# Kernel tuning notes

Hardware: AMD Instinct MI355X
Metric: run time of the kernel (lower is better)

## Reference

```python
import jax, jax.numpy as jnp
import numpy as np

B, T = 32, 64
I, O, H = 64, 64, 512
N, W = 128, 64           # memory slots, slot width
IF = 3 * W + 6           # interface size


def setup_inputs() -> dict:
    key = jax.random.key(0)
    ks = jax.random.split(key, 6)
    s = 0.05
    return {
        "x": jax.random.normal(ks[0], (B, T, I), jnp.float32),
        "W_ih": jax.random.normal(ks[1], (4 * H, I + W), jnp.float32) * s,
        "W_hh": jax.random.normal(ks[2], (4 * H, H), jnp.float32) * s,
        "b_ih": jnp.zeros((4 * H,), jnp.float32),
        "b_hh": jnp.zeros((4 * H,), jnp.float32),
        "W_if": jax.random.normal(ks[3], (IF, H), jnp.float32) * s,
        "b_if": jnp.zeros((IF,), jnp.float32),
        "W_out": jax.random.normal(ks[4], (O, H + W), jnp.float32) * s,
        "b_out": jnp.zeros((O,), jnp.float32),
    }


def reference(x, W_ih, W_hh, b_ih, b_hh, W_if, b_if, W_out, b_out):
    Bb, Tt, _ = x.shape
    dt = x.dtype
    eye = jnp.eye(N, dtype=dt)
    batch_idx = jnp.arange(Bb)[:, None]

    def step(carry, x_t):
        h, c, mem, usage, prec, link, rw, rvec = carry
        # --- LSTM controller (PyTorch gate order i,f,g,o) ---
        inp = jnp.concatenate([x_t, rvec], axis=-1)
        gates = inp @ W_ih.T + h @ W_hh.T + b_ih + b_hh
        i_g, f_g, g_g, o_g = jnp.split(gates, 4, axis=-1)
        c = jax.nn.sigmoid(f_g) * c + jax.nn.sigmoid(i_g) * jnp.tanh(g_g)
        h = jax.nn.sigmoid(o_g) * jnp.tanh(c)
        itf = h @ W_if.T + b_if
        # --- parse interface ---
        erase = jax.nn.sigmoid(itf[:, :W])
        wvec = itf[:, W:2 * W]
        wg = jax.nn.sigmoid(itf[:, 2 * W])
        ag = jax.nn.sigmoid(itf[:, 2 * W + 1])
        rstr = jnp.log1p(jnp.exp(itf[:, 3 * W + 2]))  # softplus
        # --- allocation weighting (sort usage asc, shifted cumprod, scatter) ---
        idx = jnp.argsort(usage, axis=-1)
        usage_sorted = jnp.take_along_axis(usage, idx, axis=-1)
        cprod = jnp.cumprod(usage_sorted, axis=-1)
        cprod = jnp.concatenate([jnp.ones((Bb, 1), dt), cprod[:, :-1]], axis=-1)
        alloc_in_order = (1.0 - usage_sorted) * cprod
        alloc = jnp.zeros_like(usage).at[batch_idx, idx].set(alloc_in_order)
        ww = wg[:, None] * ag[:, None] * alloc  # [B,N]
        # --- erase + add write ---
        mem = mem * (1.0 - ww[:, :, None] * erase[:, None, :]) + ww[:, :, None] * wvec[:, None, :]
        usage = usage + (1.0 - usage) * ww
        # --- temporal link / precedence ---
        ww_ij = ww[:, :, None] + ww[:, None, :]
        link = (1.0 - ww_ij) * link + prec[:, :, None] * ww[:, None, :]
        link = link * (1.0 - eye)
        prec = (1.0 - ww.sum(-1, keepdims=True)) * prec + ww
        # --- read weights (NOTE: source uses itf[:, :W] as read key) ---
        rmode = jax.nn.softmax(itf[:, -3:], axis=-1)
        rkey = itf[:, :W]
        dot = jnp.einsum('bw,bnw->bn', rkey, mem)
        kn = jnp.linalg.norm(rkey, axis=-1, keepdims=True) + 1e-8
        mn = jnp.linalg.norm(mem, axis=-1) + 1e-8
        cw = jax.nn.softmax(dot / (kn * mn) * rstr[:, None], axis=-1)
        bw = jnp.einsum('bnm,bn->bm', link, rw)   # link^T @ rw
        fw = jnp.einsum('bnm,bm->bn', link, rw)   # link @ rw
        wts = rmode[:, 0:1] * bw + rmode[:, 1:2] * fw + rmode[:, 2:3] * cw + 1e-8
        wts = wts / wts.sum(-1, keepdims=True)
        rvec = jnp.einsum('bn,bnw->bw', wts, mem)
        out = jnp.concatenate([h, rvec], axis=-1) @ W_out.T + b_out
        return (h, c, mem, usage, prec, link, wts, rvec), out

    z = lambda *s: jnp.zeros(s, dt)
    carry0 = (z(Bb, H), z(Bb, H), z(Bb, N, W), z(Bb, N), z(Bb, N), z(Bb, N, N), z(Bb, N), z(Bb, W))
    _, outs = jax.lax.scan(step, carry0, jnp.swapaxes(x, 0, 1))
    return jnp.swapaxes(outs, 0, 1)  # [B,T,O]
```

## Files before the change

### kernel.cpp

```cpp
#include <hip/hip_runtime.h>
#include <math.h>

#define Bb 32
#define Tt 64
#define Ii 64
#define Oo 64
#define Hh 512
#define Nn 128
#define Wd 64
#define IFs 198
#define KV 640
#define G4 2048

#define NP1 128
#define NWG 160
#define NT 512

#define P2_MEM    0
#define P2_H      8320
#define P2_SCR    8896
#define P2_ITF    10944
#define P2_ERASE  11168
#define P2_WVEC   11232
#define P2_USAGE  11296
#define P2_PREC   11424
#define P2_RW     11552
#define P2_WW     11680
#define P2_SCAN   11808
#define P2_SS     11936
#define P2_SCAL   12064
#define P2_BIF    12080
#define P2_ALLOC  12304
#define P1_WIF    0
#define P1_BS     13464
#define P1_V      13720
#define P1_CC     15016
#define P1_HSL    15144
#define P1_PACC   15272
#define SMEM_FLOATS 23592
#define SMEM_BYTES (SMEM_FLOATS * 4)

#define S_WWSUM 0

__device__ __align__(16) float g_WT[KV * G4];
__device__ __align__(16) float g_bsum[G4];
typedef unsigned long long u64;
__device__ u64 g_h64[2 * Bb * Hh];
__device__ u64 g_rv64[Bb * Wd];
__device__ u64 g_if64[Bb * 8 * 200];

__device__ __forceinline__ float sigf(float v) { return 1.f / (1.f + expf(-v)); }

__device__ __forceinline__ u64 ldrelax(const u64* p) {
  return __hip_atomic_load(p, __ATOMIC_RELAXED, __HIP_MEMORY_SCOPE_AGENT);
}
__device__ __forceinline__ void tstore(u64* p, unsigned tag, float v) {
  u64 val = ((u64)tag << 32) | (u64)__float_as_uint(v);
  __hip_atomic_store(p, val, __ATOMIC_RELAXED, __HIP_MEMORY_SCOPE_AGENT);
}
__device__ __forceinline__ float fixwait(const u64* p, u64 v, unsigned tag) {
  while ((unsigned)(v >> 32) != tag) {
    __builtin_amdgcn_s_sleep(1);
    v = ldrelax(p);
  }
  return __uint_as_float((unsigned)(v & 0xffffffffu));
}

#define TIN 512
__global__ __launch_bounds__(TIN) void dnc_init(const float* __restrict__ W_ih,
                                                const float* __restrict__ W_hh,
                                                const float* __restrict__ b_ih,
                                                const float* __restrict__ b_hh) {
  __shared__ float tile[64][65];
  const int tid = threadIdx.x;
  int i0 = blockIdx.x * blockDim.x + tid;
  int st = gridDim.x * blockDim.x;
  for (int idx = i0; idx < G4; idx += st) g_bsum[idx] = b_ih[idx] + b_hh[idx];
  for (int idx = i0; idx < 2 * Bb * Hh; idx += st) g_h64[idx] = 0ull;
  for (int idx = i0; idx < Bb * Wd; idx += st) g_rv64[idx] = 0ull;
  for (int idx = i0; idx < Bb * 8 * 200; idx += st) g_if64[idx] = 0ull;

  for (int tileId = blockIdx.x; tileId < 320; tileId += gridDim.x) {
    int tc = tileId >> 5, tj = tileId & 31;
    for (int k = tid; k < 64 * 64; k += TIN) {
      int r = k >> 6, cl = k & 63;
      int j = tj * 64 + r, c = tc * 64 + cl;
      tile[r][cl] = (c < 128) ? W_ih[j * 128 + c] : W_hh[j * 512 + (c - 128)];
    }
    __syncthreads();
    for (int k = tid; k < 64 * 64; k += TIN) {
      int cl = k >> 6, rjj = k & 63;
      int c = tc * 64 + cl;
      int rp = (c < 128) ? (512 + c) : (c - 128);
      g_WT[(size_t)rp * G4 + tj * 64 + rjj] = tile[rjj][cl];
    }
    __syncthreads();
  }
}

__global__ __launch_bounds__(NT) void dnc_main(const float* __restrict__ x,
                                               const float* __restrict__ W_if,
                                               const float* __restrict__ b_if,
                                               const float* __restrict__ W_out,
                                               const float* __restrict__ b_out,
                                               float* __restrict__ out) {
  extern __shared__ float sm[];
  const int tid = threadIdx.x;
  const int wg = blockIdx.x;

  if (wg < NP1) {
    const int jb = wg & 7;
    const int bb = wg >> 3;
    const int b0 = bb * 2;
    for (int i = tid; i < IFs * 64; i += NT) {
      int o = i >> 6, c = i & 63;
      sm[P1_WIF + o * 68 + c] = W_if[(size_t)o * Hh + jb * 64 + c];
    }
    if (tid < 64) {
      int gq = tid >> 4, m = tid & 15;
      ((float4*)(sm + P1_BS))[tid] = ((const float4*)g_bsum)[gq * 128 + jb * 16 + m];
    }
    if (tid < 128) sm[P1_CC + tid] = 0.f;
    __syncthreads();

    for (int t = 0; t < Tt; ++t) {
      {
        const u64* hsrc = g_h64 + (size_t)((t + 1) & 1) * (Bb * Hh);
        const int u = tid;
        const u64* a0 = hsrc + (size_t)b0 * Hh + u;
        const u64* a1 = hsrc + (size_t)(b0 + 1) * Hh + u;
        u64 v0 = ldrelax(a0), v1 = ldrelax(a1);
        float2 hh;
        hh.x = fixwait(a0, v0, (unsigned)t);
        hh.y = fixwait(a1, v1, (unsigned)t);
        *(float2*)(sm + P1_V + u * 2) = hh;
        if (tid < 128) {
          const int bl2 = tid >> 6, i = tid & 63;
          float xv = x[((size_t)(b0 + bl2) * Tt + t) * Ii + i];
          sm[P1_V + (512 + i) * 2 + bl2] = xv;
        }
      }
      __syncthreads();

      {
        const int fg = tid & 31, ks = tid >> 5;
        const int fcolA = ((fg >> 4) * 128) + jb * 16 + (fg & 15);
        const float* v2 = sm + P1_V + ks * 80;
        const float4* wpA = (const float4*)g_WT + (size_t)(ks * 40) * 512 + fcolA;
        if (ks >= 14) {
          const int j = tid & 63;
          const u64* r0 = g_rv64 + (size_t)b0 * Wd + j;
          const u64* r1 = g_rv64 + (size_t)(b0 + 1) * Wd + j;
          u64 u0 = ldrelax(r0), u1 = ldrelax(r1);
          float2 rv;
          rv.x = fixwait(r0, u0, (unsigned)t);
          rv.y = fixwait(r1, u1, (unsigned)t);
          *(float2*)(sm + P1_V + (576 + j) * 2) = rv;
        }
        float4 aA0 = {0.f, 0.f, 0.f, 0.f}, aA1 = {0.f, 0.f, 0.f, 0.f};
        float4 aB0 = {0.f, 0.f, 0.f, 0.f}, aB1 = {0.f, 0.f, 0.f, 0.f};
#pragma unroll 4
        for (int r = 0; r < 40; ++r) {
          float4 wA = wpA[(size_t)r * 512];
          float4 wB = wpA[(size_t)r * 512 + 256];
          float2 vv = *(const float2*)(v2 + r * 2);
          aA0.x += wA.x * vv.x; aA0.y += wA.y * vv.x; aA0.z += wA.z * vv.x; aA0.w += wA.w * vv.x;
          aA1.x += wA.x * vv.y; aA1.y += wA.y * vv.y; aA1.z += wA.z * vv.y; aA1.w += wA.w * vv.y;
          aB0.x += wB.x * vv.x; aB0.y += wB.y * vv.x; aB0.z += wB.z * vv.x; aB0.w += wB.w * vv.x;
          aB1.x += wB.x * vv.y; aB1.y += wB.y * vv.y; aB1.z += wB.z * vv.y; aB1.w += wB.w * vv.y;
        }
        float4* pacc = (float4*)(sm + P1_PACC);
        pacc[(ks * 2 + 0) * 65 + fg] = aA0;
        pacc[(ks * 2 + 1) * 65 + fg] = aA1;
        pacc[(ks * 2 + 0) * 65 + fg + 32] = aB0;
        pacc[(ks * 2 + 1) * 65 + fg + 32] = aB1;
      }
      __syncthreads();
      if (tid < 128) {
        const int bl = tid >> 6, l = tid & 63;
        const float* pb = sm + P1_PACC + bl * 260 + l;
        float gv0 = 0.f, gv1 = 0.f, gv2 = 0.f, gv3 = 0.f;
#pragma unroll
        for (int ks = 0; ks < 16; ++ks) {
          const float* pk = pb + ks * 520;
          gv0 += pk[0];
          gv1 += pk[64];
          gv2 += pk[128];
          gv3 += pk[192];
        }
        float ig = gv0 + sm[P1_BS + l];
        float fg = gv1 + sm[P1_BS + 64 + l];
        float gg = gv2 + sm[P1_BS + 128 + l];
        float og = gv3 + sm[P1_BS + 192 + l];
        float co = sm[P1_CC + bl * 64 + l];
        float cn = sigf(fg) * co + sigf(ig) * tanhf(gg);
        float hn = sigf(og) * tanhf(cn);
        sm[P1_CC + bl * 64 + l] = cn;
        sm[P1_HSL + bl * 64 + l] = hn;
        tstore(g_h64 + (size_t)(t & 1) * (Bb * Hh) + (size_t)(b0 + bl) * Hh + jb * 64 + l,
               (unsigned)(t + 1), hn);
      }
      __syncthreads();
      if (tid < 2 * IFs) {
        const int o = tid >> 1, bl = tid & 1;
        const float4* wr = (const float4*)(sm + P1_WIF + o * 68);
        const float4* h4 = (const float4*)(sm + P1_HSL + bl * 64);
        float acc = 0.f;
#pragma unroll 8
        for (int c4 = 0; c4 < 16; ++c4) {
          float4 w = wr[c4]; float4 h = h4[c4];
          acc += w.x * h.x + w.y * h.y + w.z * h.z + w.w * h.w;
        }
        tstore(g_if64 + ((size_t)(b0 + bl) * 8 + jb) * 200 + o, (unsigned)(t + 1), acc);
      }
    }
  } else {
    const int b = wg - NP1;
    float* SCR = sm + P2_SCR;
    float regL[32], regLT[32];
#pragma unroll
    for (int k = 0; k < 32; ++k) { regL[k] = 0.f; regLT[k] = 0.f; }
    for (int i = tid; i < Nn * 65; i += NT) sm[P2_MEM + i] = 0.f;
    if (tid < 128) { sm[P2_USAGE + tid] = 0.f; sm[P2_PREC + tid] = 0.f; sm[P2_RW + tid] = 0.f; }
    if (tid < IFs) sm[P2_BIF + tid] = b_if[tid];
    __syncthreads();
    if (tid < 64) {
      const int li = tid, i0 = 2 * li, i1 = i0 + 1;
      float u0 = sm[P2_USAGE + i0], u1 = sm[P2_USAGE + i1];
      int r0 = 0, r1 = 0;
      for (int jc = 0; jc < 32; ++jc) {
        float4 uj4 = *(const float4*)(sm + P2_USAGE + jc * 4);
#pragma unroll
        for (int e = 0; e < 4; ++e) {
          float uj = (&uj4.x)[e];
          int j = jc * 4 + e;
          r0 += (uj < u0 || (uj == u0 && j < i0)) ? 1 : 0;
          r1 += (uj < u1 || (uj == u1 && j < i1)) ? 1 : 0;
        }
      }
      sm[P2_SS + r0] = u0;
      sm[P2_SS + r1] = u1;
      float s0 = sm[P2_SS + i0], s1 = sm[P2_SS + i1];
      float p = s0 * s1;
#pragma unroll
      for (int off = 1; off < 64; off <<= 1) {
        float v = __shfl_up(p, off, 64);
        if (li >= off) p *= v;
      }
      float E = __shfl_up(p, 1, 64);
      if (li == 0) E = 1.f;
      sm[P2_SCAN + i0] = E * s0;
      sm[P2_SCAN + i1] = E * s0 * s1;
      float ex0 = (r0 > 0) ? sm[P2_SCAN + r0 - 1] : 1.f;
      float ex1 = (r1 > 0) ? sm[P2_SCAN + r1 - 1] : 1.f;
      sm[P2_ALLOC + i0] = (1.f - u0) * ex0;
      sm[P2_ALLOC + i1] = (1.f - u1) * ex1;
    }
    __syncthreads();

    for (int t = 0; t < Tt; ++t) {
      if (tid < 2 * IFs) {
        const int o = tid >> 1, hf = tid & 1;
        const u64* src = g_if64 + ((size_t)b * 8 + hf * 4) * 200 + o;
        u64 a0 = ldrelax(src), a1 = ldrelax(src + 200),
            a2 = ldrelax(src + 400), a3 = ldrelax(src + 600);
        float s = fixwait(src, a0, (unsigned)(t + 1))
                + fixwait(src + 200, a1, (unsigned)(t + 1))
                + fixwait(src + 400, a2, (unsigned)(t + 1))
                + fixwait(src + 600, a3, (unsigned)(t + 1));
        s += __shfl_xor(s, 1, 64);
        if (hf == 0) sm[P2_ITF + o] = s + sm[P2_BIF + o];
      }
      __syncthreads();
      float kn_r = 0.f, rstr_r = 0.f, rm0_r = 0.f, rm1_r = 0.f, rm2_r = 0.f;
      if (tid < 64) {
        const int li = tid, i0 = 2 * li, i1 = i0 + 1;
        float wgag = sigf(sm[P2_ITF + 128]) * sigf(sm[P2_ITF + 129]);
        float rs = sm[P2_ITF + 194];
        rstr_r = (rs > 20.f) ? rs : log1pf(expf(rs));
        float m0 = sm[P2_ITF + 195], m1 = sm[P2_ITF + 196], m2 = sm[P2_ITF + 197];
        float mx = fmaxf(m0, fmaxf(m1, m2));
        float e0 = expf(m0 - mx), e1 = expf(m1 - mx), e2 = expf(m2 - mx);
        float es = e0 + e1 + e2;
        rm0_r = e0 / es; rm1_r = e1 / es; rm2_r = e2 / es;
        float rk = sm[P2_ITF + li];
        sm[P2_ERASE + li] = sigf(rk);
        sm[P2_WVEC + li] = sm[P2_ITF + 64 + li];
        float sq = rk * rk;
#pragma unroll
        for (int off = 32; off > 0; off >>= 1) sq += __shfl_xor(sq, off, 64);
        kn_r = sqrtf(sq) + 1e-8f;
        float u0 = sm[P2_USAGE + i0], u1 = sm[P2_USAGE + i1];
        float w0 = wgag * sm[P2_ALLOC + i0];
        float w1 = wgag * sm[P2_ALLOC + i1];
        sm[P2_WW + i0] = w0; sm[P2_WW + i1] = w1;
        sm[P2_USAGE + i0] = u0 + (1.f - u0) * w0;
        sm[P2_USAGE + i1] = u1 + (1.f - u1) * w1;
        float wws = w0 + w1;
#pragma unroll
        for (int off = 32; off > 0; off >>= 1) wws += __shfl_xor(wws, off, 64);
        if (li == 0) sm[P2_SCAL + S_WWSUM] = wws;
      }
      __syncthreads();
      {
        const int n = tid & 127, ws = tid >> 7;
        float4 er[4], wv[4], kf[4];
#pragma unroll
        for (int r = 0; r < 4; ++r) {
          er[r] = *(const float4*)(sm + P2_ERASE + ws * 16 + r * 4);
          wv[r] = *(const float4*)(sm + P2_WVEC + ws * 16 + r * 4);
          kf[r] = *(const float4*)(sm + P2_ITF + ws * 16 + r * 4);
        }
        float wwn = sm[P2_WW + n];
        float dotp = 0.f, mnp = 0.f;
        const int base = P2_MEM + n * 65 + ws * 16;
#pragma unroll
        for (int q = 0; q < 16; ++q) {
          float m = sm[base + q];
          float ee = (&er[q >> 2].x)[q & 3];
          float vv = (&wv[q >> 2].x)[q & 3];
          float kk = (&kf[q >> 2].x)[q & 3];
          m = m * (1.f - wwn * ee) + wwn * vv;
          sm[base + q] = m;
          dotp += kk * m;
          mnp += m * m;
        }
        SCR[ws * 128 + n] = dotp;
        SCR[512 + ws * 128 + n] = mnp;
        const int m = n, ns = ws;
        float wwm = wwn;
        float prn = sm[P2_PREC + m];
        float bwp = 0.f, fwp = 0.f;
#pragma unroll
        for (int kq = 0; kq < 8; ++kq) {
          float4 ww4 = *(const float4*)(sm + P2_WW + ns * 32 + kq * 4);
          float4 pr4 = *(const float4*)(sm + P2_PREC + ns * 32 + kq * 4);
          float4 rw4 = *(const float4*)(sm + P2_RW + ns * 32 + kq * 4);
#pragma unroll
          for (int e = 0; e < 4; ++e) {
            int k = kq * 4 + e;
            int nn = ns * 32 + k;
            float wwo = (&ww4.x)[e];
            float pro = (&pr4.x)[e];
            float rwo = (&rw4.x)[e];
            float L = regL[k];
            L = (1.f - wwo - wwm) * L + pro * wwm;
            if (nn == m) L = 0.f;
            regL[k] = L;
            bwp += L * rwo;
            float LT = regLT[k];
            LT = (1.f - wwm - wwo) * LT + prn * wwo;
            if (nn == m) LT = 0.f;
            regLT[k] = LT;
            fwp += LT * rwo;
          }
        }
        SCR[1024 + ns * 128 + m] = bwp;
        SCR[1536 + ns * 128 + m] = fwp;
      }
      __syncthreads();
      if (tid < 64) {
        int i0 = 2 * tid, i1 = i0 + 1;
        float d0 = SCR[i0] + SCR[128 + i0] + SCR[256 + i0] + SCR[384 + i0];
        float d1 = SCR[i1] + SCR[128 + i1] + SCR[256 + i1] + SCR[384 + i1];
        float mn0 = sqrtf(SCR[512 + i0] + SCR[640 + i0] + SCR[768 + i0] + SCR[896 + i0]) + 1e-8f;
        float mn1 = sqrtf(SCR[512 + i1] + SCR[640 + i1] + SCR[768 + i1] + SCR[896 + i1]) + 1e-8f;
        float bw0 = SCR[1024 + i0] + SCR[1152 + i0] + SCR[1280 + i0] + SCR[1408 + i0];
        float bw1 = SCR[1024 + i1] + SCR[1152 + i1] + SCR[1280 + i1] + SCR[1408 + i1];
        float fw0 = SCR[1536 + i0] + SCR[1664 + i0] + SCR[1792 + i0] + SCR[1920 + i0];
        float fw1 = SCR[1536 + i1] + SCR[1664 + i1] + SCR[1792 + i1] + SCR[1920 + i1];
        float q0 = d0 / (kn_r * mn0) * rstr_r;
        float q1 = d1 / (kn_r * mn1) * rstr_r;
        float mx = fmaxf(q0, q1);
#pragma unroll
        for (int off = 32; off > 0; off >>= 1) mx = fmaxf(mx, __shfl_xor(mx, off, 64));
        float e0 = expf(q0 - mx), e1 = expf(q1 - mx);
        float es = e0 + e1;
#pragma unroll
        for (int off = 32; off > 0; off >>= 1) es += __shfl_xor(es, off, 64);
        float wv0 = rm0_r * bw0 + rm1_r * fw0 + rm2_r * (e0 / es) + 1e-8f;
        float wv1 = rm0_r * bw1 + rm1_r * fw1 + rm2_r * (e1 / es) + 1e-8f;
        float wsum = wv0 + wv1;
#pragma unroll
        for (int off = 32; off > 0; off >>= 1) wsum += __shfl_xor(wsum, off, 64);
        sm[P2_RW + i0] = wv0 / wsum;
        sm[P2_RW + i1] = wv1 / wsum;
      }
      __syncthreads();
      {
        const int w = tid & 63, ns8 = tid >> 6;
        float4 rw4[4];
#pragma unroll
        for (int r = 0; r < 4; ++r)
          rw4[r] = *(const float4*)(sm + P2_RW + ns8 * 16 + r * 4);
        float p = 0.f;
#pragma unroll
        for (int k = 0; k < 16; ++k)
          p += (&rw4[k >> 2].x)[k & 3] * sm[P2_MEM + (ns8 * 16 + k) * 65 + w];
        SCR[ns8 * 64 + w] = p;
      }
      __syncthreads();
      if (tid < 64) {
        float r = 0.f;
#pragma unroll
        for (int s2 = 0; s2 < 8; ++s2) r += SCR[s2 * 64 + tid];
        sm[P2_H + 512 + tid] = r;
        tstore(g_rv64 + (size_t)b * Wd + tid, (unsigned)(t + 1), r);
      } else if (tid < 320) {
        const int idx = tid - 64;
        const u64* hsrc = g_h64 + (size_t)(t & 1) * (Bb * Hh) + (size_t)b * Hh;
        const u64* a0 = hsrc + idx * 2;
        const u64* a1 = hsrc + idx * 2 + 1;
        u64 v0 = ldrelax(a0), v1 = ldrelax(a1);
        sm[P2_H + idx * 2] = fixwait(a0, v0, (unsigned)(t + 1));
        sm[P2_H + idx * 2 + 1] = fixwait(a1, v1, (unsigned)(t + 1));
      } else if (tid < 384) {
        const int li = tid - 320, i0 = 2 * li, i1 = i0 + 1;
        float u0 = sm[P2_USAGE + i0], u1 = sm[P2_USAGE + i1];
        int r0 = 0, r1 = 0;
        for (int jc = 0; jc < 32; ++jc) {
          float4 uj4 = *(const float4*)(sm + P2_USAGE + jc * 4);
#pragma unroll
          for (int e = 0; e < 4; ++e) {
            float uj = (&uj4.x)[e];
            int j = jc * 4 + e;
            r0 += (uj < u0 || (uj == u0 && j < i0)) ? 1 : 0;
            r1 += (uj < u1 || (uj == u1 && j < i1)) ? 1 : 0;
          }
        }
        sm[P2_SS + r0] = u0;
        sm[P2_SS + r1] = u1;
        float s0 = sm[P2_SS + i0], s1 = sm[P2_SS + i1];
        float p = s0 * s1;
#pragma unroll
        for (int off = 1; off < 64; off <<= 1) {
          float v = __shfl_up(p, off, 64);
          if (li >= off) p *= v;
        }
        float E = __shfl_up(p, 1, 64);
        if (li == 0) E = 1.f;
        sm[P2_SCAN + i0] = E * s0;
        sm[P2_SCAN + i1] = E * s0 * s1;
        float ex0 = (r0 > 0) ? sm[P2_SCAN + r0 - 1] : 1.f;
        float ex1 = (r1 > 0) ? sm[P2_SCAN + r1 - 1] : 1.f;
        sm[P2_ALLOC + i0] = (1.f - u0) * ex0;
        sm[P2_ALLOC + i1] = (1.f - u1) * ex1;
      } else {
        const int n = tid - 384;
        float wws = sm[P2_SCAL + S_WWSUM];
        sm[P2_PREC + n] = (1.f - wws) * sm[P2_PREC + n] + sm[P2_WW + n];
      }
      __syncthreads();
      {
        const int o = tid >> 3, seg = tid & 7;
        const float4* wrow = (const float4*)(W_out + (size_t)o * 576) + seg * 18;
        const float4* hb = (const float4*)(sm + P2_H) + seg * 18;
        float p = 0.f;
#pragma unroll
        for (int q = 0; q < 18; ++q) {
          float4 w = wrow[q]; float4 h = hb[q];
          p += w.x * h.x + w.y * h.y + w.z * h.z + w.w * h.w;
        }
        p += __shfl_down(p, 4, 8);
        p += __shfl_down(p, 2, 8);
        p += __shfl_down(p, 1, 8);
        if (seg == 0) out[((size_t)b * Tt + t) * Oo + o] = p + b_out[o];
      }
    }
  }
}

extern "C" void kernel_launch(void* const* d_in, const int* in_sizes, int n_in,
                              void* d_out, int out_size, void* d_ws, size_t ws_size,
                              hipStream_t stream) {
  (void)in_sizes; (void)n_in; (void)d_ws; (void)ws_size; (void)out_size;
  const float* x    = (const float*)d_in[0];
  const float* W_ih = (const float*)d_in[1];
  const float* W_hh = (const float*)d_in[2];
  const float* b_ih = (const float*)d_in[3];
  const float* b_hh = (const float*)d_in[4];
  const float* W_if = (const float*)d_in[5];
  const float* b_if = (const float*)d_in[6];
  const float* W_out = (const float*)d_in[7];
// ... 14 lines not shown
```

Baseline: 873.5 us.

## Merge memory-phase workgroups into LSTM workgroups with redundant per-batch memory state

The separate 32 memory-phase workgroups are removed. Each of the 128 controller workgroups now redundantly keeps the DNC memory, usage, precedence and link state for its two batch rows in LDS and registers. This drops the read-vector round trip through global memory and one cross-workgroup handoff per step, leaving only the h and interface-partial exchanges. The output projection is split across the 8 column workgroups and deferred by one step. In exchange, the memory update is computed eight times over, LDS use per workgroup grows, and the link matrix lives in large per-thread register arrays that may spill.

Result: slower. 2.089 ms (+139.1%).

```diff
diff --git a/kernel.cpp b/kernel.cpp
--- a/kernel.cpp
+++ b/kernel.cpp
@@ -12,41 +12,35 @@
 #define KV 640
 #define G4 2048
 
-#define NP1 128
-#define NWG 160
+#define NWG 128
 #define NT 512
 
-#define P2_MEM    0
-#define P2_H      8320
-#define P2_SCR    8896
-#define P2_ITF    10944
-#define P2_ERASE  11168
-#define P2_WVEC   11232
-#define P2_USAGE  11296
-#define P2_PREC   11424
-#define P2_RW     11552
-#define P2_WW     11680
-#define P2_SCAN   11808
-#define P2_SS     11936
-#define P2_SCAL   12064
-#define P2_BIF    12080
-#define P2_ALLOC  12304
-#define P1_WIF    0
-#define P1_BS     13464
-#define P1_V      13720
-#define P1_CC     15016
-#define P1_HSL    15144
-#define P1_PACC   15272
-#define SMEM_FLOATS 23592
+#define L_V      0
+#define L_BS     1280
+#define L_CC     1536
+#define L_HSL    1664
+#define L_BIF    1792
+#define L_ITF    2016
+#define L_ERASE  2464
+#define L_WVEC   2592
+#define L_USAGE  2720
+#define L_PREC   2976
+#define L_RW     3232
+#define L_WW     3488
+#define L_SCAN   3744
+#define L_SS     4000
+#define L_ALLOC  4256
+#define L_SCAL   4512
+#define L_SCR    4544
+#define L_PACC   6592
+#define L_MEM    14912
+#define SMEM_FLOATS 31552
 #define SMEM_BYTES (SMEM_FLOATS * 4)
-
-#define S_WWSUM 0
 
 __device__ __align__(16) float g_WT[KV * G4];
 __device__ __align__(16) float g_bsum[G4];
 typedef unsigned long long u64;
 __device__ u64 g_h64[2 * Bb * Hh];
-__device__ u64 g_rv64[Bb * Wd];
 __device__ u64 g_if64[Bb * 8 * 200];
 
 __device__ __forceinline__ float sigf(float v) { return 1.f / (1.f + expf(-v)); }
@@ -77,7 +71,6 @@
   int st = gridDim.x * blockDim.x;
   for (int idx = i0; idx < G4; idx += st) g_bsum[idx] = b_ih[idx] + b_hh[idx];
   for (int idx = i0; idx < 2 * Bb * Hh; idx += st) g_h64[idx] = 0ull;
-  for (int idx = i0; idx < Bb * Wd; idx += st) g_rv64[idx] = 0ull;
   for (int idx = i0; idx < Bb * 8 * 200; idx += st) g_if64[idx] = 0ull;
 
   for (int tileId = blockIdx.x; tileId < 320; tileId += gridDim.x) {
@@ -98,248 +91,289 @@
   }
 }
 
-__global__ __launch_bounds__(NT) void dnc_main(const float* __restrict__ x,
-                                               const float* __restrict__ W_if,
-                                               const float* __restrict__ b_if,
-                                               const float* __restrict__ W_out,
-                                               const float* __restrict__ b_out,
-                                               float* __restrict__ out) {
+__global__ __launch_bounds__(NT, 2) void dnc_main(const float* __restrict__ x,
+                                                  const float* __restrict__ W_if,
+                                                  const float* __restrict__ b_if,
+                                                  const float* __restrict__ W_out,
+                                                  const float* __restrict__ b_out,
+                                                  float* __restrict__ out) {
   extern __shared__ float sm[];
   const int tid = threadIdx.x;
   const int wg = blockIdx.x;
-
-  if (wg < NP1) {
-    const int jb = wg & 7;
-    const int bb = wg >> 3;
-    const int b0 = bb * 2;
-    for (int i = tid; i < IFs * 64; i += NT) {
-      int o = i >> 6, c = i & 63;
-      sm[P1_WIF + o * 68 + c] = W_if[(size_t)o * Hh + jb * 64 + c];
-    }
-    if (tid < 64) {
-      int gq = tid >> 4, m = tid & 15;
-      ((float4*)(sm + P1_BS))[tid] = ((const float4*)g_bsum)[gq * 128 + jb * 16 + m];
-    }
-    if (tid < 128) sm[P1_CC + tid] = 0.f;
-    __syncthreads();
-
-    for (int t = 0; t < Tt; ++t) {
+  const int jb = wg & 7;
+  const int bb = wg >> 3;
+  const int b0 = bb * 2;
+
+  float regL[64], regLT[64];
+#pragma unroll
+  for (int k = 0; k < 64; ++k) { regL[k] = 0.f; regLT[k] = 0.f; }
+
+  if (tid < 64) {
+    int gq = tid >> 4, m = tid & 15;
+    ((float4*)(sm + L_BS))[tid] = ((const float4*)g_bsum)[gq * 128 + jb * 16 + m];
+  }
+  if (tid < 128) {
+    sm[L_CC + tid] = 0.f;
+    sm[L_V + (576 + (tid & 63)) * 2 + (tid >> 6)] = 0.f;
+  }
+  if (tid < IFs) sm[L_BIF + tid] = b_if[tid];
+  if (tid < 256) {
+    int bl = tid >> 7, n = tid & 127;
+    sm[L_USAGE + bl * 128 + n] = 0.f;
+    sm[L_PREC + bl * 128 + n] = 0.f;
+    sm[L_RW + bl * 128 + n] = 0.f;
+  }
+  for (int i = tid; i < 2 * Nn * 65; i += NT) sm[L_MEM + i] = 0.f;
+  __syncthreads();
+  if (tid < 128) {
+    const int bl = tid >> 6, li = tid & 63, i0 = 2 * li, i1 = i0 + 1;
+    float* USb = sm + L_USAGE + bl * 128;
+    float* SSb = sm + L_SS + bl * 128;
+    float* SCb = sm + L_SCAN + bl * 128;
+    float* ALb = sm + L_ALLOC + bl * 128;
+    float u0 = USb[i0], u1 = USb[i1];
+    int r0 = 0, r1 = 0;
+    for (int jc = 0; jc < 32; ++jc) {
+      float4 uj4 = *(const float4*)(USb + jc * 4);
+#pragma unroll
+      for (int e = 0; e < 4; ++e) {
+        float uj = (&uj4.x)[e];
+        int j = jc * 4 + e;
+        r0 += (uj < u0 || (uj == u0 && j < i0)) ? 1 : 0;
+        r1 += (uj < u1 || (uj == u1 && j < i1)) ? 1 : 0;
+      }
+    }
+    SSb[r0] = u0;
+    SSb[r1] = u1;
+    float s0 = SSb[i0], s1 = SSb[i1];
+    float p = s0 * s1;
+#pragma unroll
+    for (int off = 1; off < 64; off <<= 1) {
+      float v = __shfl_up(p, off, 64);
+      if (li >= off) p *= v;
+    }
+    float E = __shfl_up(p, 1, 64);
+    if (li == 0) E = 1.f;
+    SCb[i0] = E * s0;
+    SCb[i1] = E * s0 * s1;
+    float ex0 = (r0 > 0) ? SCb[r0 - 1] : 1.f;
+    float ex1 = (r1 > 0) ? SCb[r1 - 1] : 1.f;
+    ALb[i0] = (1.f - u0) * ex0;
+    ALb[i1] = (1.f - u1) * ex1;
+  }
+  __syncthreads();
+
+  for (int t = 0; t < Tt; ++t) {
+    {
+      const u64* hsrc = g_h64 + (size_t)((t + 1) & 1) * (Bb * Hh);
+      const int u = tid;
+      const u64* a0 = hsrc + (size_t)b0 * Hh + u;
+      const u64* a1 = hsrc + (size_t)(b0 + 1) * Hh + u;
+      u64 v0 = ldrelax(a0), v1 = ldrelax(a1);
+      float2 hh;
+      hh.x = fixwait(a0, v0, (unsigned)t);
+      hh.y = fixwait(a1, v1, (unsigned)t);
+      *(float2*)(sm + L_V + u * 2) = hh;
+      if (tid < 128) {
+        const int bl2 = tid >> 6, i = tid & 63;
+        sm[L_V + (512 + i) * 2 + bl2] = x[((size_t)(b0 + bl2) * Tt + t) * Ii + i];
+      }
+    }
+    __syncthreads();
+    {
+      const int fg = tid & 31, ks = tid >> 5;
+      const int fcolA = ((fg >> 4) * 128) + jb * 16 + (fg & 15);
+      const float* v2 = sm + L_V + ks * 80;
+      const float4* wpA = (const float4*)g_WT + (size_t)(ks * 40) * 512 + fcolA;
+      float4 aA0 = {0.f, 0.f, 0.f, 0.f}, aA1 = {0.f, 0.f, 0.f, 0.f};
+      float4 aB0 = {0.f, 0.f, 0.f, 0.f}, aB1 = {0.f, 0.f, 0.f, 0.f};
+#pragma unroll 4
+      for (int r = 0; r < 40; ++r) {
+        float4 wA = wpA[(size_t)r * 512];
+        float4 wB = wpA[(size_t)r * 512 + 256];
+        float2 vv = *(const float2*)(v2 + r * 2);
+        aA0.x += wA.x * vv.x; aA0.y += wA.y * vv.x; aA0.z += wA.z * vv.x; aA0.w += wA.w * vv.x;
+        aA1.x += wA.x * vv.y; aA1.y += wA.y * vv.y; aA1.z += wA.z * vv.y; aA1.w += wA.w * vv.y;
+        aB0.x += wB.x * vv.x; aB0.y += wB.y * vv.x; aB0.z += wB.z * vv.x; aB0.w += wB.w * vv.x;
+        aB1.x += wB.x * vv.y; aB1.y += wB.y * vv.y; aB1.z += wB.z * vv.y; aB1.w += wB.w * vv.y;
+      }
+      float4* pacc = (float4*)(sm + L_PACC);
+      pacc[(ks * 2 + 0) * 65 + fg] = aA0;
+      pacc[(ks * 2 + 1) * 65 + fg] = aA1;
+      pacc[(ks * 2 + 0) * 65 + fg + 32] = aB0;
+      pacc[(ks * 2 + 1) * 65 + fg + 32] = aB1;
+    }
+    __syncthreads();
+    if (tid < 128) {
+      const int bl = tid >> 6, l = tid & 63;
+      const float* pb = sm + L_PACC + bl * 260 + l;
+      float gv0 = 0.f, gv1 = 0.f, gv2 = 0.f, gv3 = 0.f;
+#pragma unroll
+      for (int ks = 0; ks < 16; ++ks) {
+        const float* pk = pb + ks * 520;
+        gv0 += pk[0];
+        gv1 += pk[64];
+        gv2 += pk[128];
+        gv3 += pk[192];
+      }
+      float ig = gv0 + sm[L_BS + l];
+      float fg = gv1 + sm[L_BS + 64 + l];
+      float gg = gv2 + sm[L_BS + 128 + l];
+      float og = gv3 + sm[L_BS + 192 + l];
+      float co = sm[L_CC + bl * 64 + l];
+      float cn = sigf(fg) * co + sigf(ig) * tanhf(gg);
+      float hn = sigf(og) * tanhf(cn);
+      sm[L_CC + bl * 64 + l] = cn;
+      sm[L_HSL + bl * 64 + l] = hn;
+      tstore(g_h64 + (size_t)(t & 1) * (Bb * Hh) + (size_t)(b0 + bl) * Hh + jb * 64 + l,
+             (unsigned)(t + 1), hn);
+    }
+    __syncthreads();
+    if (tid < 2 * IFs) {
+      const int o = tid >> 1, bl = tid & 1;
+      const float4* wr = (const float4*)(W_if + (size_t)o * Hh + jb * 64);
+      const float4* h4 = (const float4*)(sm + L_HSL + bl * 64);
+      float acc = 0.f;
+#pragma unroll 8
+      for (int c4 = 0; c4 < 16; ++c4) {
+        float4 w = wr[c4]; float4 h = h4[c4];
+        acc += w.x * h.x + w.y * h.y + w.z * h.z + w.w * h.w;
+      }
+      tstore(g_if64 + ((size_t)(b0 + bl) * 8 + jb) * 200 + o, (unsigned)(t + 1), acc);
+    }
+    const u64* pp0; const u64* pp1; const u64* pp2; const u64* pp3;
+    const u64* pp4; const u64* pp5; const u64* pp6; const u64* pp7;
+    u64 pv0 = 0, pv1 = 0, pv2 = 0, pv3 = 0, pv4 = 0, pv5 = 0, pv6 = 0, pv7 = 0;
+    if (tid < 2 * IFs) {
+      const int o = tid >> 1, bl = tid & 1;
+      const u64* base = g_if64 + (size_t)(b0 + bl) * 8 * 200 + o;
+      pp0 = base;        pp1 = base + 200;  pp2 = base + 400;  pp3 = base + 600;
+      pp4 = base + 800;  pp5 = base + 1000; pp6 = base + 1200; pp7 = base + 1400;
+      pv0 = ldrelax(pp0); pv1 = ldrelax(pp1); pv2 = ldrelax(pp2); pv3 = ldrelax(pp3);
+      pv4 = ldrelax(pp4); pv5 = ldrelax(pp5); pv6 = ldrelax(pp6); pv7 = ldrelax(pp7);
+    }
+    if (t > 0 && tid < 256) {
+      const int g = tid >> 4, seg = tid & 15;
+      const int o = jb * 8 + (g >> 1), bl = g & 1;
+      const float4* w4 = (const float4*)(W_out + (size_t)o * 576) + seg * 9;
+      float p = 0.f;
+#pragma unroll
+      for (int q = 0; q < 9; ++q) {
+        float4 w = w4[q];
+        int v = seg * 36 + q * 4;
+        int r0 = (v < 512) ? v : v + 64;
+        p += w.x * sm[L_V + (r0 + 0) * 2 + bl];
+        p += w.y * sm[L_V + (r0 + 1) * 2 + bl];
+        p += w.z * sm[L_V + (r0 + 2) * 2 + bl];
+        p += w.w * sm[L_V + (r0 + 3) * 2 + bl];
+      }
+      p += __shfl_down(p, 8, 16);
+      p += __shfl_down(p, 4, 16);
+      p += __shfl_down(p, 2, 16);
+      p += __shfl_down(p, 1, 16);
+      if (seg == 0) out[((size_t)(b0 + bl) * Tt + (t - 1)) * Oo + o] = p + b_out[o];
+    }
+    if (tid < 2 * IFs) {
+      const int o = tid >> 1, bl = tid & 1;
+      float sA = fixwait(pp0, pv0, (unsigned)(t + 1))
+               + fixwait(pp1, pv1, (unsigned)(t + 1))
+               + fixwait(pp2, pv2, (unsigned)(t + 1))
+               + fixwait(pp3, pv3, (unsigned)(t + 1));
+      float sB = fixwait(pp4, pv4, (unsigned)(t + 1))
+               + fixwait(pp5, pv5, (unsigned)(t + 1))
+               + fixwait(pp6, pv6, (unsigned)(t + 1))
+               + fixwait(pp7, pv7, (unsigned)(t + 1));
+      sm[L_ITF + bl * 224 + o] = (sA + sB) + sm[L_BIF + o];
+    }
+    __syncthreads();
+    float kn_r = 0.f, rstr_r = 0.f, rm0_r = 0.f, rm1_r = 0.f, rm2_r = 0.f;
+    if (tid < 128) {
+      const int bl = tid >> 6, li = tid & 63, i0 = 2 * li, i1 = i0 + 1;
+      const float* ITFb = sm + L_ITF + bl * 224;
+      float wgag = sigf(ITFb[128]) * sigf(ITFb[129]);
+      float rs = ITFb[194];
+      rstr_r = (rs > 20.f) ? rs : log1pf(expf(rs));
+      float m0 = ITFb[195], m1 = ITFb[196], m2 = ITFb[197];
+      float mx = fmaxf(m0, fmaxf(m1, m2));
+      float e0 = expf(m0 - mx), e1 = expf(m1 - mx), e2 = expf(m2 - mx);
+      float es = e0 + e1 + e2;
+      rm0_r = e0 / es; rm1_r = e1 / es; rm2_r = e2 / es;
+      float rk = ITFb[li];
+      sm[L_ERASE + bl * 64 + li] = sigf(rk);
+      sm[L_WVEC + bl * 64 + li] = ITFb[64 + li];
+      float sq = rk * rk;
+#pragma unroll
+      for (int off = 32; off > 0; off >>= 1) sq += __shfl_xor(sq, off, 64);
+      kn_r = sqrtf(sq) + 1e-8f;
+      float* USb = sm + L_USAGE + bl * 128;
+      float* WWb = sm + L_WW + bl * 128;
+      const float* ALb = sm + L_ALLOC + bl * 128;
+      float u0 = USb[i0], u1 = USb[i1];
+      float w0 = wgag * ALb[i0];
+      float w1 = wgag * ALb[i1];
+      WWb[i0] = w0; WWb[i1] = w1;
+      USb[i0] = u0 + (1.f - u0) * w0;
+      USb[i1] = u1 + (1.f - u1) * w1;
+      float wws = w0 + w1;
+#pragma unroll
+      for (int off = 32; off > 0; off >>= 1) wws += __shfl_xor(wws, off, 64);
+      if (li == 0) sm[L_SCAL + bl * 16] = wws;
+    }
+    __syncthreads();
+    {
+      const int bl = tid >> 8, s = tid & 255;
+      float* MEMb = sm + L_MEM + bl * 8320;
+      float* SCRb = sm + L_SCR + bl * 1024;
+      const float* WWb = sm + L_WW + bl * 128;
       {
-        const u64* hsrc = g_h64 + (size_t)((t + 1) & 1) * (Bb * Hh);
-        const int u = tid;
-        const u64* a0 = hsrc + (size_t)b0 * Hh + u;
-        const u64* a1 = hsrc + (size_t)(b0 + 1) * Hh + u;
-        u64 v0 = ldrelax(a0), v1 = ldrelax(a1);
-        float2 hh;
-        hh.x = fixwait(a0, v0, (unsigned)t);
-        hh.y = fixwait(a1, v1, (unsigned)t);
-        *(float2*)(sm + P1_V + u * 2) = hh;
-        if (tid < 128) {
-          const int bl2 = tid >> 6, i = tid & 63;
-          float xv = x[((size_t)(b0 + bl2) * Tt + t) * Ii + i];
-          sm[P1_V + (512 + i) * 2 + bl2] = xv;
+        const int n = s & 127, ws2 = s >> 7;
+        const float* ERb = sm + L_ERASE + bl * 64 + ws2 * 32;
+        const float* WVb = sm + L_WVEC + bl * 64 + ws2 * 32;
+        const float* KFb = sm + L_ITF + bl * 224 + ws2 * 32;
+        float wwn = WWb[n];
+        float dotp = 0.f, mnp = 0.f;
+        const int mbase = n * 65 + ws2 * 32;
+#pragma unroll
+        for (int hq = 0; hq < 2; ++hq) {
+          float4 er[4], wv[4], kf[4];
+#pragma unroll
+          for (int r = 0; r < 4; ++r) {
+            er[r] = *(const float4*)(ERb + hq * 16 + r * 4);
+            wv[r] = *(const float4*)(WVb + hq * 16 + r * 4);
+            kf[r] = *(const float4*)(KFb + hq * 16 + r * 4);
+          }
+#pragma unroll
+          for (int q = 0; q < 16; ++q) {
+            float m = MEMb[mbase + hq * 16 + q];
+            float ee = (&er[q >> 2].x)[q & 3];
+            float vv = (&wv[q >> 2].x)[q & 3];
+            float kk = (&kf[q >> 2].x)[q & 3];
+            m = m * (1.f - wwn * ee) + wwn * vv;
+            MEMb[mbase + hq * 16 + q] = m;
+            dotp += kk * m;
+            mnp += m * m;
+          }
         }
-      }
-      __syncthreads();
-
+        SCRb[ws2 * 128 + n] = dotp;
+        SCRb[256 + ws2 * 128 + n] = mnp;
+      }
       {
-        const int fg = tid & 31, ks = tid >> 5;
-        const int fcolA = ((fg >> 4) * 128) + jb * 16 + (fg & 15);
-        const float* v2 = sm + P1_V + ks * 80;
-        const float4* wpA = (const float4*)g_WT + (size_t)(ks * 40) * 512 + fcolA;
-        if (ks >= 14) {
-          const int j = tid & 63;
-          const u64* r0 = g_rv64 + (size_t)b0 * Wd + j;
-          const u64* r1 = g_rv64 + (size_t)(b0 + 1) * Wd + j;
-          u64 u0 = ldrelax(r0), u1 = ldrelax(r1);
-          float2 rv;
-          rv.x = fixwait(r0, u0, (unsigned)t);
-          rv.y = fixwait(r1, u1, (unsigned)t);
-          *(float2*)(sm + P1_V + (576 + j) * 2) = rv;
-        }
-        float4 aA0 = {0.f, 0.f, 0.f, 0.f}, aA1 = {0.f, 0.f, 0.f, 0.f};
-        float4 aB0 = {0.f, 0.f, 0.f, 0.f}, aB1 = {0.f, 0.f, 0.f, 0.f};
-#pragma unroll 4
-        for (int r = 0; r < 40; ++r) {
-          float4 wA = wpA[(size_t)r * 512];
-          float4 wB = wpA[(size_t)r * 512 + 256];
-          float2 vv = *(const float2*)(v2 + r * 2);
-          aA0.x += wA.x * vv.x; aA0.y += wA.y * vv.x; aA0.z += wA.z * vv.x; aA0.w += wA.w * vv.x;
-          aA1.x += wA.x * vv.y; aA1.y += wA.y * vv.y; aA1.z += wA.z * vv.y; aA1.w += wA.w * vv.y;
-          aB0.x += wB.x * vv.x; aB0.y += wB.y * vv.x; aB0.z += wB.z * vv.x; aB0.w += wB.w * vv.x;
-          aB1.x += wB.x * vv.y; aB1.y += wB.y * vv.y; aB1.z += wB.z * vv.y; aB1.w += wB.w * vv.y;
-        }
-        float4* pacc = (float4*)(sm + P1_PACC);
-        pacc[(ks * 2 + 0) * 65 + fg] = aA0;
-        pacc[(ks * 2 + 1) * 65 + fg] = aA1;
-        pacc[(ks * 2 + 0) * 65 + fg + 32] = aB0;
-        pacc[(ks * 2 + 1) * 65 + fg + 32] = aB1;
-      }
-      __syncthreads();
-      if (tid < 128) {
-        const int bl = tid >> 6, l = tid & 63;
-        const float* pb = sm + P1_PACC + bl * 260 + l;
-        float gv0 = 0.f, gv1 = 0.f, gv2 = 0.f, gv3 = 0.f;
-#pragma unroll
-        for (int ks = 0; ks < 16; ++ks) {
-          const float* pk = pb + ks * 520;
-          gv0 += pk[0];
-          gv1 += pk[64];
-          gv2 += pk[128];
-          gv3 += pk[192];
-        }
-        float ig = gv0 + sm[P1_BS + l];
-        float fg = gv1 + sm[P1_BS + 64 + l];
-        float gg = gv2 + sm[P1_BS + 128 + l];
-        float og = gv3 + sm[P1_BS + 192 + l];
-        float co = sm[P1_CC + bl * 64 + l];
-        float cn = sigf(fg) * co + sigf(ig) * tanhf(gg);
-        float hn = sigf(og) * tanhf(cn);
-        sm[P1_CC + bl * 64 + l] = cn;
-        sm[P1_HSL + bl * 64 + l] = hn;
-        tstore(g_h64 + (size_t)(t & 1) * (Bb * Hh) + (size_t)(b0 + bl) * Hh + jb * 64 + l,
-               (unsigned)(t + 1), hn);
-      }
-      __syncthreads();
-      if (tid < 2 * IFs) {
-        const int o = tid >> 1, bl = tid & 1;
-        const float4* wr = (const float4*)(sm + P1_WIF + o * 68);
-        const float4* h4 = (const float4*)(sm + P1_HSL + bl * 64);
-        float acc = 0.f;
-#pragma unroll 8
-        for (int c4 = 0; c4 < 16; ++c4) {
-          float4 w = wr[c4]; float4 h = h4[c4];
-          acc += w.x * h.x + w.y * h.y + w.z * h.z + w.w * h.w;
-        }
-        tstore(g_if64 + ((size_t)(b0 + bl) * 8 + jb) * 200 + o, (unsigned)(t + 1), acc);
-      }
-    }
-  } else {
-    const int b = wg - NP1;
-    float* SCR = sm + P2_SCR;
-    float regL[32], regLT[32];
-#pragma unroll
-    for (int k = 0; k < 32; ++k) { regL[k] = 0.f; regLT[k] = 0.f; }
-    for (int i = tid; i < Nn * 65; i += NT) sm[P2_MEM + i] = 0.f;
-    if (tid < 128) { sm[P2_USAGE + tid] = 0.f; sm[P2_PREC + tid] = 0.f; sm[P2_RW + tid] = 0.f; }
-    if (tid < IFs) sm[P2_BIF + tid] = b_if[tid];
-    __syncthreads();
-    if (tid < 64) {
-      const int li = tid, i0 = 2 * li, i1 = i0 + 1;
-      float u0 = sm[P2_USAGE + i0], u1 = sm[P2_USAGE + i1];
-      int r0 = 0, r1 = 0;
-      for (int jc = 0; jc < 32; ++jc) {
-        float4 uj4 = *(const float4*)(sm + P2_USAGE + jc * 4);
-#pragma unroll
-        for (int e = 0; e < 4; ++e) {
-          float uj = (&uj4.x)[e];
-          int j = jc * 4 + e;
-          r0 += (uj < u0 || (uj == u0 && j < i0)) ? 1 : 0;
-          r1 += (uj < u1 || (uj == u1 && j < i1)) ? 1 : 0;
-        }
-      }
-      sm[P2_SS + r0] = u0;
-      sm[P2_SS + r1] = u1;
-      float s0 = sm[P2_SS + i0], s1 = sm[P2_SS + i1];
-      float p = s0 * s1;
-#pragma unroll
-      for (int off = 1; off < 64; off <<= 1) {
-        float v = __shfl_up(p, off, 64);
-        if (li >= off) p *= v;
-      }
-      float E = __shfl_up(p, 1, 64);
-      if (li == 0) E = 1.f;
-      sm[P2_SCAN + i0] = E * s0;
-      sm[P2_SCAN + i1] = E * s0 * s1;
-      float ex0 = (r0 > 0) ? sm[P2_SCAN + r0 - 1] : 1.f;
-      float ex1 = (r1 > 0) ? sm[P2_SCAN + r1 - 1] : 1.f;
-      sm[P2_ALLOC + i0] = (1.f - u0) * ex0;
-      sm[P2_ALLOC + i1] = (1.f - u1) * ex1;
-    }
-    __syncthreads();
-
-    for (int t = 0; t < Tt; ++t) {
-      if (tid < 2 * IFs) {
-        const int o = tid >> 1, hf = tid & 1;
-        const u64* src = g_if64 + ((size_t)b * 8 + hf * 4) * 200 + o;
-        u64 a0 = ldrelax(src), a1 = ldrelax(src + 200),
-            a2 = ldrelax(src + 400), a3 = ldrelax(src + 600);
-        float s = fixwait(src, a0, (unsigned)(t + 1))
-                + fixwait(src + 200, a1, (unsigned)(t + 1))
-                + fixwait(src + 400, a2, (unsigned)(t + 1))
-                + fixwait(src + 600, a3, (unsigned)(t + 1));
-        s += __shfl_xor(s, 1, 64);
-        if (hf == 0) sm[P2_ITF + o] = s + sm[P2_BIF + o];
-      }
-      __syncthreads();
-      float kn_r = 0.f, rstr_r = 0.f, rm0_r = 0.f, rm1_r = 0.f, rm2_r = 0.f;
-      if (tid < 64) {
-        const int li = tid, i0 = 2 * li, i1 = i0 + 1;
-        float wgag = sigf(sm[P2_ITF + 128]) * sigf(sm[P2_ITF + 129]);
-        float rs = sm[P2_ITF + 194];
-        rstr_r = (rs > 20.f) ? rs : log1pf(expf(rs));
-        float m0 = sm[P2_ITF + 195], m1 = sm[P2_ITF + 196], m2 = sm[P2_ITF + 197];
-        float mx = fmaxf(m0, fmaxf(m1, m2));
-        float e0 = expf(m0 - mx), e1 = expf(m1 - mx), e2 = expf(m2 - mx);
-        float es = e0 + e1 + e2;
-        rm0_r = e0 / es; rm1_r = e1 / es; rm2_r = e2 / es;
-        float rk = sm[P2_ITF + li];
-        sm[P2_ERASE + li] = sigf(rk);
-        sm[P2_WVEC + li] = sm[P2_ITF + 64 + li];
-        float sq = rk * rk;
-#pragma unroll
-        for (int off = 32; off > 0; off >>= 1) sq += __shfl_xor(sq, off, 64);
-        kn_r = sqrtf(sq) + 1e-8f;
-        float u0 = sm[P2_USAGE + i0], u1 = sm[P2_USAGE + i1];
-        float w0 = wgag * sm[P2_ALLOC + i0];
-        float w1 = wgag * sm[P2_ALLOC + i1];
-        sm[P2_WW + i0] = w0; sm[P2_WW + i1] = w1;
-        sm[P2_USAGE + i0] = u0 + (1.f - u0) * w0;
-        sm[P2_USAGE + i1] = u1 + (1.f - u1) * w1;
-        float wws = w0 + w1;
-#pragma unroll
-        for (int off = 32; off > 0; off >>= 1) wws += __shfl_xor(wws, off, 64);
-        if (li == 0) sm[P2_SCAL + S_WWSUM] = wws;
-      }
-      __syncthreads();
-      {
-        const int n = tid & 127, ws = tid >> 7;
-        float4 er[4], wv[4], kf[4];
-#pragma unroll
-        for (int r = 0; r < 4; ++r) {
-          er[r] = *(const float4*)(sm + P2_ERASE + ws * 16 + r * 4);
-          wv[r] = *(const float4*)(sm + P2_WVEC + ws * 16 + r * 4);
-          kf[r] = *(const float4*)(sm + P2_ITF + ws * 16 + r * 4);
-        }
-        float wwn = sm[P2_WW + n];
-        float dotp = 0.f, mnp = 0.f;
-        const int base = P2_MEM + n * 65 + ws * 16;
-#pragma unroll
-        for (int q = 0; q < 16; ++q) {
-          float m = sm[base + q];
-          float ee = (&er[q >> 2].x)[q & 3];
-          float vv = (&wv[q >> 2].x)[q & 3];
-          float kk = (&kf[q >> 2].x)[q & 3];
-          m = m * (1.f - wwn * ee) + wwn * vv;
-          sm[base + q] = m;
-          dotp += kk * m;
-          mnp += m * m;
-        }
-        SCR[ws * 128 + n] = dotp;
-        SCR[512 + ws * 128 + n] = mnp;
-        const int m = n, ns = ws;
-        float wwm = wwn;
-        float prn = sm[P2_PREC + m];
+        const int m = s & 127, kh = s >> 7;
+        const float* WWh = sm + L_WW + bl * 128 + kh * 64;
+        const float* PRh = sm + L_PREC + bl * 128 + kh * 64;
+        const float* RWh = sm + L_RW + bl * 128 + kh * 64;
+        float wwm = (sm + L_WW + bl * 128)[m];
+        float prn = (sm + L_PREC + bl * 128)[m];
         float bwp = 0.f, fwp = 0.f;
 #pragma unroll
-        for (int kq = 0; kq < 8; ++kq) {
-          float4 ww4 = *(const float4*)(sm + P2_WW + ns * 32 + kq * 4);
-          float4 pr4 = *(const float4*)(sm + P2_PREC + ns * 32 + kq * 4);
-          float4 rw4 = *(const float4*)(sm + P2_RW + ns * 32 + kq * 4);
+        for (int kq = 0; kq < 16; ++kq) {
+          float4 ww4 = *(const float4*)(WWh + kq * 4);
+          float4 pr4 = *(const float4*)(PRh + kq * 4);
+          float4 rw4 = *(const float4*)(RWh + kq * 4);
 #pragma unroll
           for (int e = 0; e < 4; ++e) {
             int k = kq * 4 + e;
-            int nn = ns * 32 + k;
+            int nn = kh * 64 + k;
             float wwo = (&ww4.x)[e];
             float pro = (&pr4.x)[e];
             float rwo = (&rw4.x)[e];
@@ -355,118 +389,138 @@
             fwp += LT * rwo;
           }
         }
-        SCR[1024 + ns * 128 + m] = bwp;
-        SCR[1536 + ns * 128 + m] = fwp;
-      }
-      __syncthreads();
-      if (tid < 64) {
-        int i0 = 2 * tid, i1 = i0 + 1;
-        float d0 = SCR[i0] + SCR[128 + i0] + SCR[256 + i0] + SCR[384 + i0];
-        float d1 = SCR[i1] + SCR[128 + i1] + SCR[256 + i1] + SCR[384 + i1];
-        float mn0 = sqrtf(SCR[512 + i0] + SCR[640 + i0] + SCR[768 + i0] + SCR[896 + i0]) + 1e-8f;
-        float mn1 = sqrtf(SCR[512 + i1] + SCR[640 + i1] + SCR[768 + i1] + SCR[896 + i1]) + 1e-8f;
-        float bw0 = SCR[1024 + i0] + SCR[1152 + i0] + SCR[1280 + i0] + SCR[1408 + i0];
-        float bw1 = SCR[1024 + i1] + SCR[1152 + i1] + SCR[1280 + i1] + SCR[1408 + i1];
-        float fw0 = SCR[1536 + i0] + SCR[1664 + i0] + SCR[1792 + i0] + SCR[1920 + i0];
-        float fw1 = SCR[1536 + i1] + SCR[1664 + i1] + SCR[1792 + i1] + SCR[1920 + i1];
-        float q0 = d0 / (kn_r * mn0) * rstr_r;
-        float q1 = d1 / (kn_r * mn1) * rstr_r;
-        float mx = fmaxf(q0, q1);
-#pragma unroll
-        for (int off = 32; off > 0; off >>= 1) mx = fmaxf(mx, __shfl_xor(mx, off, 64));
-        float e0 = expf(q0 - mx), e1 = expf(q1 - mx);
-        float es = e0 + e1;
-#pragma unroll
-        for (int off = 32; off > 0; off >>= 1) es += __shfl_xor(es, off, 64);
-        float wv0 = rm0_r * bw0 + rm1_r * fw0 + rm2_r * (e0 / es) + 1e-8f;
-        float wv1 = rm0_r * bw1 + rm1_r * fw1 + rm2_r * (e1 / es) + 1e-8f;
-        float wsum = wv0 + wv1;
-#pragma unroll
-        for (int off = 32; off > 0; off >>= 1) wsum += __shfl_xor(wsum, off, 64);
-        sm[P2_RW + i0] = wv0 / wsum;
-        sm[P2_RW + i1] = wv1 / wsum;
-      }
-      __syncthreads();
-      {
-        const int w = tid & 63, ns8 = tid >> 6;
-        float4 rw4[4];
-#pragma unroll
-        for (int r = 0; r < 4; ++r)
-          rw4[r] = *(const float4*)(sm + P2_RW + ns8 * 16 + r * 4);
-        float p = 0.f;
-#pragma unroll
-        for (int k = 0; k < 16; ++k)
-          p += (&rw4[k >> 2].x)[k & 3] * sm[P2_MEM + (ns8 * 16 + k) * 65 + w];
-        SCR[ns8 * 64 + w] = p;
-      }
-      __syncthreads();
-      if (tid < 64) {
-        float r = 0.f;
-#pragma unroll
-        for (int s2 = 0; s2 < 8; ++s2) r += SCR[s2 * 64 + tid];
-        sm[P2_H + 512 + tid] = r;
-        tstore(g_rv64 + (size_t)b * Wd + tid, (unsigned)(t + 1), r);
-      } else if (tid < 320) {
-        const int idx = tid - 64;
-        const u64* hsrc = g_h64 + (size_t)(t & 1) * (Bb * Hh) + (size_t)b * Hh;
-        const u64* a0 = hsrc + idx * 2;
-        const u64* a1 = hsrc + idx * 2 + 1;
-        u64 v0 = ldrelax(a0), v1 = ldrelax(a1);
-        sm[P2_H + idx * 2] = fixwait(a0, v0, (unsigned)(t + 1));
-        sm[P2_H + idx * 2 + 1] = fixwait(a1, v1, (unsigned)(t + 1));
-      } else if (tid < 384) {
-        const int li = tid - 320, i0 = 2 * li, i1 = i0 + 1;
-        float u0 = sm[P2_USAGE + i0], u1 = sm[P2_USAGE + i1];
-        int r0 = 0, r1 = 0;
-        for (int jc = 0; jc < 32; ++jc) {
-          float4 uj4 = *(const float4*)(sm + P2_USAGE + jc * 4);
-#pragma unroll
-          for (int e = 0; e < 4; ++e) {
-            float uj = (&uj4.x)[e];
-            int j = jc * 4 + e;
-            r0 += (uj < u0 || (uj == u0 && j < i0)) ? 1 : 0;
-            r1 += (uj < u1 || (uj == u1 && j < i1)) ? 1 : 0;
-          }
+        SCRb[512 + kh * 128 + m] = bwp;
+        SCRb[768 + kh * 128 + m] = fwp;
+      }
+    }
+    __syncthreads();
+    if (tid < 128) {
+      const int bl = tid >> 6, li = tid & 63;
+      const float* SCRb = sm + L_SCR + bl * 1024;
+      int i0 = 2 * li, i1 = i0 + 1;
+      float d0 = SCRb[i0] + SCRb[128 + i0];
+      float d1 = SCRb[i1] + SCRb[128 + i1];
+      float mn0 = sqrtf(SCRb[256 + i0] + SCRb[384 + i0]) + 1e-8f;
+      float mn1 = sqrtf(SCRb[256 + i1] + SCRb[384 + i1]) + 1e-8f;
+      float bw0 = SCRb[512 + i0] + SCRb[640 + i0];
+      float bw1 = SCRb[512 + i1] + SCRb[640 + i1];
+      float fw0 = SCRb[768 + i0] + SCRb[896 + i0];
+      float fw1 = SCRb[768 + i1] + SCRb[896 + i1];
+      float q0 = d0 / (kn_r * mn0) * rstr_r;
+      float q1 = d1 / (kn_r * mn1) * rstr_r;
+      float mx = fmaxf(q0, q1);
+#pragma unroll
+      for (int off = 32; off > 0; off >>= 1) mx = fmaxf(mx, __shfl_xor(mx, off, 64));
+      float e0 = expf(q0 - mx), e1 = expf(q1 - mx);
+      float es = e0 + e1;
+#pragma unroll
+      for (int off = 32; off > 0; off >>= 1) es += __shfl_xor(es, off, 64);
+      float wv0 = rm0_r * bw0 + rm1_r * fw0 + rm2_r * (e0 / es) + 1e-8f;
+      float wv1 = rm0_r * bw1 + rm1_r * fw1 + rm2_r * (e1 / es) + 1e-8f;
+      float wsum = wv0 + wv1;
+#pragma unroll
+      for (int off = 32; off > 0; off >>= 1) wsum += __shfl_xor(wsum, off, 64);
+      sm[L_RW + bl * 128 + i0] = wv0 / wsum;
+      sm[L_RW + bl * 128 + i1] = wv1 / wsum;
+    }
+    __syncthreads();
+    {
+      const int bl = tid >> 8, s = tid & 255;
+      const int w = s & 63, ns4 = s >> 6;
+      const float* MEMb = sm + L_MEM + bl * 8320;
+      const float* RWb = sm + L_RW + bl * 128;
+      float* SCRb = sm + L_SCR + bl * 1024;
+      float4 rw4[8];
+#pragma unroll
+      for (int r = 0; r < 8; ++r)
+        rw4[r] = *(const float4*)(RWb + ns4 * 32 + r * 4);
+      float p = 0.f;
+#pragma unroll
+      for (int k = 0; k < 32; ++k)
+        p += (&rw4[k >> 2].x)[k & 3] * MEMb[(ns4 * 32 + k) * 65 + w];
+      SCRb[ns4 * 64 + w] = p;
+    }
+    __syncthreads();
+    if (tid < 128) {
+      const int bl = tid >> 6, w = tid & 63;
+      const float* SCRb = sm + L_SCR + bl * 1024;
+      float r = SCRb[w] + SCRb[64 + w] + SCRb[128 + w] + SCRb[192 + w];
+      sm[L_V + (576 + w) * 2 + bl] = r;
+    } else if (tid < 256) {
+      const int bl = (tid >> 6) & 1, li = tid & 63, i0 = 2 * li, i1 = i0 + 1;
+      float* USb = sm + L_USAGE + bl * 128;
+      float* SSb = sm + L_SS + bl * 128;
+      float* SCb = sm + L_SCAN + bl * 128;
+      float* ALb = sm + L_ALLOC + bl * 128;
+      float u0 = USb[i0], u1 = USb[i1];
+      int r0 = 0, r1 = 0;
+      for (int jc = 0; jc < 32; ++jc) {
+        float4 uj4 = *(const float4*)(USb + jc * 4);
+#pragma unroll
+        for (int e = 0; e < 4; ++e) {
+          float uj = (&uj4.x)[e];
+          int j = jc * 4 + e;
+          r0 += (uj < u0 || (uj == u0 && j < i0)) ? 1 : 0;
+          r1 += (uj < u1 || (uj == u1 && j < i1)) ? 1 : 0;
         }
-        sm[P2_SS + r0] = u0;
-        sm[P2_SS + r1] = u1;
-        float s0 = sm[P2_SS + i0], s1 = sm[P2_SS + i1];
-        float p = s0 * s1;
-#pragma unroll
-        for (int off = 1; off < 64; off <<= 1) {
-          float v = __shfl_up(p, off, 64);
-          if (li >= off) p *= v;
-        }
-        float E = __shfl_up(p, 1, 64);
-        if (li == 0) E = 1.f;
-        sm[P2_SCAN + i0] = E * s0;
-        sm[P2_SCAN + i1] = E * s0 * s1;
-        float ex0 = (r0 > 0) ? sm[P2_SCAN + r0 - 1] : 1.f;
-        float ex1 = (r1 > 0) ? sm[P2_SCAN + r1 - 1] : 1.f;
-        sm[P2_ALLOC + i0] = (1.f - u0) * ex0;
-        sm[P2_ALLOC + i1] = (1.f - u1) * ex1;
-      } else {
-        const int n = tid - 384;
-        float wws = sm[P2_SCAL + S_WWSUM];
-        sm[P2_PREC + n] = (1.f - wws) * sm[P2_PREC + n] + sm[P2_WW + n];
-      }
-      __syncthreads();
-      {
-        const int o = tid >> 3, seg = tid & 7;
-        const float4* wrow = (const float4*)(W_out + (size_t)o * 576) + seg * 18;
-        const float4* hb = (const float4*)(sm + P2_H) + seg * 18;
-        float p = 0.f;
-#pragma unroll
-        for (int q = 0; q < 18; ++q) {
-          float4 w = wrow[q]; float4 h = hb[q];
-          p += w.x * h.x + w.y * h.y + w.z * h.z + w.w * h.w;
-        }
-        p += __shfl_down(p, 4, 8);
-        p += __shfl_down(p, 2, 8);
-        p += __shfl_down(p, 1, 8);
-        if (seg == 0) out[((size_t)b * Tt + t) * Oo + o] = p + b_out[o];
-      }
-    }
+      }
+      SSb[r0] = u0;
+      SSb[r1] = u1;
+      float s0 = SSb[i0], s1 = SSb[i1];
+      float p = s0 * s1;
+#pragma unroll
+      for (int off = 1; off < 64; off <<= 1) {
+        float v = __shfl_up(p, off, 64);
+        if (li >= off) p *= v;
+      }
+      float E = __shfl_up(p, 1, 64);
+      if (li == 0) E = 1.f;
+      SCb[i0] = E * s0;
+      SCb[i1] = E * s0 * s1;
+      float ex0 = (r0 > 0) ? SCb[r0 - 1] : 1.f;
+      float ex1 = (r1 > 0) ? SCb[r1 - 1] : 1.f;
+      ALb[i0] = (1.f - u0) * ex0;
+      ALb[i1] = (1.f - u1) * ex1;
+    } else {
+      const int bl = (tid >> 7) & 1, n = tid & 127;
+      float wws = sm[L_SCAL + bl * 16];
+      sm[L_PREC + bl * 128 + n] =
+          (1.f - wws) * sm[L_PREC + bl * 128 + n] + sm[L_WW + bl * 128 + n];
+    }
+    __syncthreads();
+  }
+  {
+    const u64* hsrc = g_h64 + (size_t)((Tt + 1) & 1) * (Bb * Hh);
+    const int u = tid;
+    const u64* a0 = hsrc + (size_t)b0 * Hh + u;
+    const u64* a1 = hsrc + (size_t)(b0 + 1) * Hh + u;
+    u64 v0 = ldrelax(a0), v1 = ldrelax(a1);
+    float2 hh;
+    hh.x = fixwait(a0, v0, (unsigned)Tt);
+    hh.y = fixwait(a1, v1, (unsigned)Tt);
+    *(float2*)(sm + L_V + u * 2) = hh;
+  }
+  __syncthreads();
+  if (tid < 256) {
+    const int g = tid >> 4, seg = tid & 15;
+    const int o = jb * 8 + (g >> 1), bl = g & 1;
+    const float4* w4 = (const float4*)(W_out + (size_t)o * 576) + seg * 9;
+    float p = 0.f;
+#pragma unroll
+    for (int q = 0; q < 9; ++q) {
+      float4 w = w4[q];
+      int v = seg * 36 + q * 4;
+      int r0 = (v < 512) ? v : v + 64;
+      p += w.x * sm[L_V + (r0 + 0) * 2 + bl];
+      p += w.y * sm[L_V + (r0 + 1) * 2 + bl];
+      p += w.z * sm[L_V + (r0 + 2) * 2 + bl];
+      p += w.w * sm[L_V + (r0 + 3) * 2 + bl];
+    }
+    p += __shfl_down(p, 8, 16);
+    p += __shfl_down(p, 4, 16);
+    p += __shfl_down(p, 2, 16);
+    p += __shfl_down(p, 1, 16);
+    if (seg == 0) out[((size_t)(b0 + bl) * Tt + (Tt - 1)) * Oo + o] = p + b_out[o];
   }
 }
 
```
